# Performance work log

Hardware: AMD Instinct MI355X
Metric: run time of the kernel (lower is better)

The kernel has to match this reference:

```python
import jax, jax.numpy as jnp
import numpy as np
import math

# ---- static configuration (matches init_kwargs) ----
METADATA = [64, 48, 32]   # channels per l = 0,1,2
MAX_L = 3                 # order_out
N_BATCH = 32768
fact = math.factorial

def _cg_complex(l1, m1, l2, m2, l3, m3):
    # Clebsch-Gordan coefficient <l1 m1 l2 m2 | l3 m3> via Racah formula
    if m1 + m2 != m3 or l3 < abs(l1 - l2) or l3 > l1 + l2:
        return 0.0
    pre = math.sqrt((2*l3+1) * fact(l1+l2-l3) * fact(l1-l2+l3) * fact(-l1+l2+l3) / fact(l1+l2+l3+1))
    pre *= math.sqrt(fact(l1+m1)*fact(l1-m1)*fact(l2+m2)*fact(l2-m2)*fact(l3+m3)*fact(l3-m3))
    kmin = max(0, l2-l3-m1, l1-l3+m2)
    kmax = min(l1+l2-l3, l1-m1, l2+m2)
    s = 0.0
    for k in range(kmin, kmax+1):
        s += (-1)**k / (fact(k)*fact(l1+l2-l3-k)*fact(l1-m1-k)*fact(l2+m2-k)*fact(l3-l2+m1+k)*fact(l3-l1-m2+k))
    return pre * s

def _U(l):
    # complex->real spherical harmonic change of basis, rows = real m', cols = complex m
    U = np.zeros((2*l+1, 2*l+1), dtype=np.complex128)
    for m in range(-l, l+1):
        r = m + l
        if m > 0:
            U[r, m+l] = (-1)**m / math.sqrt(2.0); U[r, -m+l] = 1.0/math.sqrt(2.0)
        elif m == 0:
            U[r, l] = 1.0
        else:
            U[r, m+l] = 1j/math.sqrt(2.0); U[r, -m+l] = -1j*(-1)**m/math.sqrt(2.0)
    return U

def _real_cg(l1, l2, l3):
    Cc = np.zeros((2*l1+1, 2*l2+1, 2*l3+1))
    for m1 in range(-l1, l1+1):
        for m2 in range(-l2, l2+1):
            for m3 in range(-l3, l3+1):
                Cc[m1+l1, m2+l2, m3+l3] = _cg_complex(l1, m1, l2, m2, l3, m3)
    T = np.einsum('am,bn,co,mno->abc', _U(l1), _U(l2), _U(l3).conj(), Cc.astype(np.complex128))
    T = T.imag if np.abs(T.imag).max() > np.abs(T.real).max() else T.real
    return np.ascontiguousarray(T).astype(np.float32)

# ---- static index structures ----
L_IN = len(METADATA)
OFF_IN = np.concatenate([[0], np.cumsum([METADATA[l]*(2*l+1) for l in range(L_IN)])]).astype(np.int64)
DIM_IN = int(OFF_IN[-1])  # 368
PATHS = []
for l1 in range(L_IN):
    for l2 in range(L_IN):
        for l3 in range(abs(l1-l2), min(l1+l2, MAX_L)+1):
            PATHS.append((l1, l2, l3, min(METADATA[l1], METADATA[l2])))
MD_OV = [0]*(MAX_L+1)
for (_, _, l3, ch) in PATHS:
    MD_OV[l3] = max(MD_OV[l3], ch)
OFF_OUT = np.concatenate([[0], np.cumsum([MD_OV[l]*(2*l+1) for l in range(MAX_L+1)])]).astype(np.int64)
DIM_OUT = int(OFF_OUT[-1])  # 672
CG = {(l1, l2, l3): jnp.asarray(_real_cg(l1, l2, l3)) for (l1, l2, l3, _) in PATHS}

_mix_id, _scat = [], []
_base = 0
for (l1, l2, l3, ch) in PATHS:
    for i in range(ch):
        for m in range(2*l3+1):
            _mix_id.append(_base + i)
            _scat.append(int(OFF_OUT[l3]) + i*(2*l3+1) + m)
    _base += ch
MIX_ID = jnp.asarray(np.array(_mix_id, dtype=np.int64))
SCATTER = jnp.asarray(np.array(_scat, dtype=np.int64))
N_MIX = _base  # 688

_chan_in = []
_cb = 0
for l in range(L_IN):
    for i in range(METADATA[l]):
        _chan_in += [_cb + i]*(2*l+1)
    _cb += METADATA[l]
CHAN_IN = jnp.asarray(np.array(_chan_in, dtype=np.int64))
N_KEEP = _cb  # 144
_kin, _kout = [], []
for l in range(L_IN):
    cp = min(METADATA[l], MD_OV[l])
    for i in range(cp):
        for m in range(2*l+1):
            _kin.append(int(OFF_IN[l]) + i*(2*l+1) + m)
            _kout.append(int(OFF_OUT[l]) + i*(2*l+1) + m)
KEEP_IN = jnp.asarray(np.array(_kin, dtype=np.int64))
KEEP_OUT = jnp.asarray(np.array(_kout, dtype=np.int64))

SQ3 = math.sqrt(3.0)

def setup_inputs() -> dict:
    key = jax.random.key(0)
    k1, k2, k3 = jax.random.split(key, 3)
    x = jax.random.normal(k1, (N_BATCH, DIM_IN), dtype=jnp.float32)
    keep_coeff = jax.random.uniform(k2, (N_KEEP,), minval=-SQ3, maxval=SQ3, dtype=jnp.float32)
    mix_coeff = jax.random.uniform(k3, (N_MIX,), minval=-SQ3, maxval=SQ3, dtype=jnp.float32)
    return {"x": x, "keep_coeff": keep_coeff, "mix_coeff": mix_coeff}

def reference(x, keep_coeff, mix_coeff):
    n = x.shape[0]
    # keep path: per-channel coeff broadcast over m components
    x_keep = x * keep_coeff[CHAN_IN]  # [N, 368]
    # CG tensor-product self-coupling (diagonal channel pairing per path)
    tps = []
    for (l1, l2, l3, ch) in PATHS:
        x1 = x[:, OFF_IN[l1]:OFF_IN[l1]+ch*(2*l1+1)].reshape(n, ch, 2*l1+1)
        x2 = x[:, OFF_IN[l2]:OFF_IN[l2]+ch*(2*l2+1)].reshape(n, ch, 2*l2+1)
        tps.append(jnp.einsum('nia,nib,abm->nim', x1, x2, CG[(l1, l2, l3)]).reshape(n, -1))
    cat = jnp.concatenate(tps, axis=1)  # [N, 2576] non-overlapped TP output
    cat = cat * 0.5 * mix_coeff[MIX_ID]
    # scatter (index_add) into overlapped output layout
    out = jnp.zeros((n, DIM_OUT), dtype=x.dtype).at[:, SCATTER].add(cat)
    # gather + add of keep path (index_select + add_)
    out = out.at[:, KEEP_OUT].add(x_keep[:, KEEP_IN])
    return out
```

## Files before the change

### kernel.cpp

```cpp
#include <hip/hip_runtime.h>


namespace cgc {

struct cplx { double re, im; };
constexpr cplx cmul(cplx a, cplx b){ return {a.re*b.re - a.im*b.im, a.re*b.im + a.im*b.re}; }

constexpr double cfact(int n){ double r = 1.0; for (int i = 2; i <= n; ++i) r *= i; return r; }
constexpr double cabsd(double x){ return x < 0 ? -x : x; }

constexpr double csqrtd(double x){
  if (x <= 0.0) return 0.0;
  double g = x > 1.0 ? x : 1.0;
  for (int i = 0; i < 48; ++i) g = 0.5*(g + x/g);
  return g;
}

constexpr double SQRT2 = csqrtd(2.0);

constexpr double cg_complex(int l1,int m1,int l2,int m2,int l3,int m3){
  if (m1 + m2 != m3) return 0.0;
  int lo = l1 > l2 ? l1 - l2 : l2 - l1;
  if (l3 < lo || l3 > l1 + l2) return 0.0;
  double pre = csqrtd((2*l3+1) * cfact(l1+l2-l3)*cfact(l1-l2+l3)*cfact(-l1+l2+l3)/cfact(l1+l2+l3+1));
  pre *= csqrtd(cfact(l1+m1)*cfact(l1-m1)*cfact(l2+m2)*cfact(l2-m2)*cfact(l3+m3)*cfact(l3-m3));
  int kmin = 0;
  if (l2-l3-m1 > kmin) kmin = l2-l3-m1;
  if (l1-l3+m2 > kmin) kmin = l1-l3+m2;
  int kmax = l1+l2-l3;
  if (l1-m1 < kmax) kmax = l1-m1;
  if (l2+m2 < kmax) kmax = l2+m2;
  double s = 0.0;
  for (int k = kmin; k <= kmax; ++k){
    double d = cfact(k)*cfact(l1+l2-l3-k)*cfact(l1-m1-k)*cfact(l2+m2-k)
             * cfact(l3-l2+m1+k)*cfact(l3-l1-m2+k);
    s += ((k & 1) ? -1.0 : 1.0) / d;
  }
  return pre * s;
}

constexpr cplx Uent(int l, int r, int c){
  int m = r - l;
  if (m > 0){
    if (c ==  m + l) return { ((m & 1) ? -1.0 : 1.0)/SQRT2, 0.0 };
    if (c == -m + l) return { 1.0/SQRT2, 0.0 };
    return {0.0, 0.0};
  } else if (m == 0){
    if (c == l) return {1.0, 0.0};
    return {0.0, 0.0};
  } else {
    int ma = -m;
    if (c ==  m + l) return { 0.0, 1.0/SQRT2 };
    if (c == -m + l) return { 0.0, -(((ma & 1) ? -1.0 : 1.0))/SQRT2 };
    return {0.0, 0.0};
  }
}

template<int L1,int L2,int L3>
struct CGData { float w[(2*L1+1)*(2*L2+1)*(2*L3+1)]; };

template<int L1,int L2,int L3>
constexpr CGData<L1,L2,L3> make_cg(){
  constexpr int D1 = 2*L1+1, D2 = 2*L2+1, D3 = 2*L3+1;
  cplx U1[D1*D1] = {}; cplx U2[D2*D2] = {}; cplx U3c[D3*D3] = {};
  for (int r = 0; r < D1; ++r) for (int c = 0; c < D1; ++c) U1[r*D1+c] = Uent(L1, r, c);
  for (int r = 0; r < D2; ++r) for (int c = 0; c < D2; ++c) U2[r*D2+c] = Uent(L2, r, c);
  for (int r = 0; r < D3; ++r) for (int c = 0; c < D3; ++c){
    cplx u = Uent(L3, r, c); u.im = -u.im; U3c[r*D3+c] = u;
  }
  double Cc[D1*D2*D3] = {};
  for (int m1 = -L1; m1 <= L1; ++m1)
    for (int m2 = -L2; m2 <= L2; ++m2){
      int m3 = m1 + m2;
      if (m3 < -L3 || m3 > L3) continue;
      Cc[((m1+L1)*D2 + (m2+L2))*D3 + (m3+L3)] = cg_complex(L1,m1,L2,m2,L3,m3);
    }
  double re[D1*D2*D3] = {}; double im[D1*D2*D3] = {};
  for (int a = 0; a < D1; ++a)
    for (int b = 0; b < D2; ++b)
      for (int c = 0; c < D3; ++c){
        double sre = 0.0, sim = 0.0;
        for (int m = 0; m < D1; ++m)
          for (int n = 0; n < D2; ++n){
            int o = m + n - L1 - L2 + L3;
            if (o < 0 || o >= D3) continue;
            double cc = Cc[(m*D2+n)*D3 + o];
            if (cc == 0.0) continue;
            cplx p = cmul(cmul(U1[a*D1+m], U2[b*D2+n]), U3c[c*D3+o]);
            sre += p.re * cc; sim += p.im * cc;
          }
        re[(a*D2+b)*D3+c] = sre; im[(a*D2+b)*D3+c] = sim;
      }
  double mre = 0.0, mim = 0.0;
  for (int k = 0; k < D1*D2*D3; ++k){
    if (cabsd(re[k]) > mre) mre = cabsd(re[k]);
    if (cabsd(im[k]) > mim) mim = cabsd(im[k]);
  }
  CGData<L1,L2,L3> outv{};
  for (int k = 0; k < D1*D2*D3; ++k){
    double v = (mim > mre) ? im[k] : re[k];
    outv.w[k] = (cabsd(v) < 1e-10) ? 0.0f : (float)v;
  }
  return outv;
}

}

template<int L1,int L2,int L3>
__device__ __forceinline__ void tp_path(const float* xa, const float* xb, float cmix, float* acc){
  constexpr cgc::CGData<L1,L2,L3> cg = cgc::make_cg<L1,L2,L3>();
  constexpr int D1 = 2*L1+1, D2 = 2*L2+1, D3 = 2*L3+1;
  #pragma unroll
  for (int a = 0; a < D1; ++a){
    #pragma unroll
    for (int b = 0; b < D2; ++b){
      const float pr = xa[a] * xb[b];
      #pragma unroll
      for (int m = 0; m < D3; ++m){
        const float W = cg.w[(a*D2+b)*D3 + m];
        if (W != 0.0f) acc[m] += (cmix * W) * pr;
      }
    }
  }
}


#define ROWS_PER_BLOCK 4

__global__ __launch_bounds__(256) void selfmix_kernel(
    const float* __restrict__ x, const float* __restrict__ keep,
    const float* __restrict__ mix, float* __restrict__ out, int n)
{
  __shared__ __align__(16) float xs[ROWS_PER_BLOCK * 368];
  __shared__ __align__(16) float os[ROWS_PER_BLOCK * 672];

  const int t = threadIdx.x;
  const long long blk  = blockIdx.x;
  const long long row0 = blk * ROWS_PER_BLOCK;

  {
    const long long nf4_in   = (long long)n * 92;
    const long long base_in  = blk * (ROWS_PER_BLOCK * 92);
    const float4* __restrict__ src = (const float4*)x;
    float4* dst = (float4*)xs;
    if (base_in + t < nf4_in)               dst[t]       = src[base_in + t];
    if (t < 112 && base_in + 256 + t < nf4_in) dst[256+t] = src[base_in + 256 + t];
  }
  __syncthreads();

  if (t < 128){
    const int rowL = t >> 5;
    const int i    = t & 31;
    if (row0 + rowL < n){
      const float* xr = xs + rowL*368;
      float*     orow = os + rowL*672;
      float s = xr[i];
      float p[3], d[5];
      #pragma unroll
      for (int k = 0; k < 3; ++k) p[k] = xr[64 + i*3 + k];
      #pragma unroll
      for (int k = 0; k < 5; ++k) d[k] = xr[208 + i*5 + k];

      float o0 = 0.f;
      float o1[3] = {0.f,0.f,0.f};
      float o2[5] = {0.f,0.f,0.f,0.f,0.f};
      float o3[7] = {0.f,0.f,0.f,0.f,0.f,0.f,0.f};

      tp_path<0,0,0>(&s,&s, 0.5f*mix[  0+i], &o0);
      tp_path<0,1,1>(&s, p, 0.5f*mix[ 64+i],  o1);
      tp_path<0,2,2>(&s, d, 0.5f*mix[112+i],  o2);
      tp_path<1,0,1>( p,&s, 0.5f*mix[144+i],  o1);
      tp_path<1,1,0>( p, p, 0.5f*mix[192+i], &o0);
      tp_path<1,1,1>( p, p, 0.5f*mix[240+i],  o1);
      tp_path<1,1,2>( p, p, 0.5f*mix[288+i],  o2);
      tp_path<1,2,1>( p, d, 0.5f*mix[336+i],  o1);
      tp_path<1,2,2>( p, d, 0.5f*mix[368+i],  o2);
      tp_path<1,2,3>( p, d, 0.5f*mix[400+i],  o3);
      tp_path<2,0,2>( d,&s, 0.5f*mix[432+i],  o2);
      tp_path<2,1,1>( d, p, 0.5f*mix[464+i],  o1);
      tp_path<2,1,2>( d, p, 0.5f*mix[496+i],  o2);
      tp_path<2,1,3>( d, p, 0.5f*mix[528+i],  o3);
      tp_path<2,2,0>( d, d, 0.5f*mix[560+i], &o0);
      tp_path<2,2,1>( d, d, 0.5f*mix[592+i],  o1);
      tp_path<2,2,2>( d, d, 0.5f*mix[624+i],  o2);
      tp_path<2,2,3>( d, d, 0.5f*mix[656+i],  o3);

      o0 += keep[i] * s;
      const float k1 = keep[64+i], k2 = keep[112+i];
      #pragma unroll
      for (int k = 0; k < 3; ++k) o1[k] += k1 * p[k];
      #pragma unroll
      for (int k = 0; k < 5; ++k) o2[k] += k2 * d[k];

      orow[i] = o0;
      #pragma unroll
      for (int k = 0; k < 3; ++k) orow[ 64 + i*3 + k] = o1[k];
      #pragma unroll
      for (int k = 0; k < 5; ++k) orow[208 + i*5 + k] = o2[k];
      #pragma unroll
      for (int k = 0; k < 7; ++k) orow[448 + i*7 + k] = o3[k];
    }
  } else if (t < 192){
    const int rowL = (t - 128) >> 4;
    const int i    = 32 + (t & 15);
    if (row0 + rowL < n){
      const float* xr = xs + rowL*368;
      float*     orow = os + rowL*672;
      float s = xr[i];
      float p[3];
      #pragma unroll
      for (int k = 0; k < 3; ++k) p[k] = xr[64 + i*3 + k];

      float o0 = 0.f;
      float o1[3] = {0.f,0.f,0.f};
      float o2[5] = {0.f,0.f,0.f,0.f,0.f};

      tp_path<0,0,0>(&s,&s, 0.5f*mix[  0+i], &o0);
      tp_path<0,1,1>(&s, p, 0.5f*mix[ 64+i],  o1);
      tp_path<1,0,1>( p,&s, 0.5f*mix[144+i],  o1);
      tp_path<1,1,0>( p, p, 0.5f*mix[192+i], &o0);
      tp_path<1,1,1>( p, p, 0.5f*mix[240+i],  o1);
      tp_path<1,1,2>( p, p, 0.5f*mix[288+i],  o2);

      o0 += keep[i] * s;
      const float k1 = keep[64+i];
      #pragma unroll
      for (int k = 0; k < 3; ++k) o1[k] += k1 * p[k];

      orow[i] = o0;
      #pragma unroll
      for (int k = 0; k < 3; ++k) orow[ 64 + i*3 + k] = o1[k];
      #pragma unroll
      for (int k = 0; k < 5; ++k) orow[208 + i*5 + k] = o2[k];
    }
  } else {
    const int rowL = (t - 192) >> 4;
    const int i    = 48 + (t & 15);
    if (row0 + rowL < n){
      const float* xr = xs + rowL*368;
      float s = xr[i];
      float o0 = 0.f;
      tp_path<0,0,0>(&s,&s, 0.5f*mix[0+i], &o0);
      o0 += keep[i] * s;
      os[rowL*672 + i] = o0;
    }
  }
  __syncthreads();

  {
    const long long nf4_out  = (long long)n * 168;
    const long long base_out = blk * (ROWS_PER_BLOCK * 168);
    const float4* srco = (const float4*)os;
    float4* __restrict__ dsto = (float4*)out;
    if (base_out + t < nf4_out)                 dsto[base_out + t]       = srco[t];
    if (base_out + 256 + t < nf4_out)           dsto[base_out + 256 + t] = srco[256+t];
    if (t < 160 && base_out + 512 + t < nf4_out) dsto[base_out + 512 + t] = srco[512+t];
  }
}

extern "C" void kernel_launch(void* const* d_in, const int* in_sizes, int n_in,
                              void* d_out, int out_size, void* d_ws, size_t ws_size,
                              hipStream_t stream)
{
  const float* x    = (const float*)d_in[0];
  const float* keep = (const float*)d_in[1];
  const float* mix  = (const float*)d_in[2];
  float* out = (float*)d_out;
  const int n = in_sizes[0] / 368;
  const int blocks = (n + ROWS_PER_BLOCK - 1) / ROWS_PER_BLOCK;
  selfmix_kernel<<<blocks, 256, 0, stream>>>(x, keep, mix, out, n);
}
```

Baseline: 147.3 us.

## Process eight rows per block with balanced thread roles and factored mix scaling

Each block now handles 8 rows instead of 4. Every thread computes one heavy channel (0-31) of one row, then also takes a lighter channel (32-47 or 48-63), so no thread idles. This replaces the old split where only 128 of 256 threads did the heavy work. tp_path now accumulates CG-weighted products into a temporary and multiplies by the mix coefficient once per output component, cutting multiplies. The cost is larger shared memory per block (about 33KB), which can limit occupancy, and per-thread work grows.

```diff
diff --git a/kernel.cpp b/kernel.cpp
--- a/kernel.cpp
+++ b/kernel.cpp
@@ -110,6 +110,9 @@
 __device__ __forceinline__ void tp_path(const float* xa, const float* xb, float cmix, float* acc){
   constexpr cgc::CGData<L1,L2,L3> cg = cgc::make_cg<L1,L2,L3>();
   constexpr int D1 = 2*L1+1, D2 = 2*L2+1, D3 = 2*L3+1;
+  float tmp[D3];
+  #pragma unroll
+  for (int m = 0; m < D3; ++m) tmp[m] = 0.0f;
   #pragma unroll
   for (int a = 0; a < D1; ++a){
     #pragma unroll
@@ -118,42 +121,45 @@
       #pragma unroll
       for (int m = 0; m < D3; ++m){
         const float W = cg.w[(a*D2+b)*D3 + m];
-        if (W != 0.0f) acc[m] += (cmix * W) * pr;
+        if (W != 0.0f) tmp[m] += W * pr;
       }
     }
   }
-}
-
-
-#define ROWS_PER_BLOCK 4
+  #pragma unroll
+  for (int m = 0; m < D3; ++m) acc[m] += cmix * tmp[m];
+}
+
+
+#define RPB 8
 
 __global__ __launch_bounds__(256) void selfmix_kernel(
     const float* __restrict__ x, const float* __restrict__ keep,
     const float* __restrict__ mix, float* __restrict__ out, int n)
 {
-  __shared__ __align__(16) float xs[ROWS_PER_BLOCK * 368];
-  __shared__ __align__(16) float os[ROWS_PER_BLOCK * 672];
+  __shared__ __align__(16) float xs[RPB * 368];
+  __shared__ __align__(16) float os[RPB * 672];
 
   const int t = threadIdx.x;
   const long long blk  = blockIdx.x;
-  const long long row0 = blk * ROWS_PER_BLOCK;
+  const long long row0 = blk * RPB;
 
   {
-    const long long nf4_in   = (long long)n * 92;
-    const long long base_in  = blk * (ROWS_PER_BLOCK * 92);
-    const float4* __restrict__ src = (const float4*)x;
-    float4* dst = (float4*)xs;
-    if (base_in + t < nf4_in)               dst[t]       = src[base_in + t];
-    if (t < 112 && base_in + 256 + t < nf4_in) dst[256+t] = src[base_in + 256 + t];
+    const long long nf4  = (long long)n * 92;
+    const long long base = row0 * 92;
+    const float4* __restrict__ x4 = (const float4*)x;
+    float4* xs4 = (float4*)xs;
+    if (base + t < nf4)                   xs4[t]       = x4[base + t];
+    if (base + 256 + t < nf4)             xs4[256 + t] = x4[base + 256 + t];
+    if (t < 224 && base + 512 + t < nf4)  xs4[512 + t] = x4[base + 512 + t];
   }
   __syncthreads();
 
-  if (t < 128){
+  {
     const int rowL = t >> 5;
     const int i    = t & 31;
     if (row0 + rowL < n){
-      const float* xr = xs + rowL*368;
-      float*     orow = os + rowL*672;
+      const float* xr = xs + rowL * 368;
+      float*     orw  = os + rowL * 672;
       float s = xr[i];
       float p[3], d[5];
       #pragma unroll
@@ -192,20 +198,22 @@
       #pragma unroll
       for (int k = 0; k < 5; ++k) o2[k] += k2 * d[k];
 
-      orow[i] = o0;
-      #pragma unroll
-      for (int k = 0; k < 3; ++k) orow[ 64 + i*3 + k] = o1[k];
-      #pragma unroll
-      for (int k = 0; k < 5; ++k) orow[208 + i*5 + k] = o2[k];
-      #pragma unroll
-      for (int k = 0; k < 7; ++k) orow[448 + i*7 + k] = o3[k];
-    }
-  } else if (t < 192){
-    const int rowL = (t - 128) >> 4;
+      orw[i] = o0;
+      #pragma unroll
+      for (int k = 0; k < 3; ++k) orw[ 64 + i*3 + k] = o1[k];
+      #pragma unroll
+      for (int k = 0; k < 5; ++k) orw[208 + i*5 + k] = o2[k];
+      #pragma unroll
+      for (int k = 0; k < 7; ++k) orw[448 + i*7 + k] = o3[k];
+    }
+  }
+
+  if (t < 128){
+    const int rowL = t >> 4;
     const int i    = 32 + (t & 15);
     if (row0 + rowL < n){
-      const float* xr = xs + rowL*368;
-      float*     orow = os + rowL*672;
+      const float* xr = xs + rowL * 368;
+      float*     orw  = os + rowL * 672;
       float s = xr[i];
       float p[3];
       #pragma unroll
@@ -227,18 +235,18 @@
       #pragma unroll
       for (int k = 0; k < 3; ++k) o1[k] += k1 * p[k];
 
-      orow[i] = o0;
-      #pragma unroll
-      for (int k = 0; k < 3; ++k) orow[ 64 + i*3 + k] = o1[k];
-      #pragma unroll
-      for (int k = 0; k < 5; ++k) orow[208 + i*5 + k] = o2[k];
+      orw[i] = o0;
+      #pragma unroll
+      for (int k = 0; k < 3; ++k) orw[ 64 + i*3 + k] = o1[k];
+      #pragma unroll
+      for (int k = 0; k < 5; ++k) orw[208 + i*5 + k] = o2[k];
     }
   } else {
-    const int rowL = (t - 192) >> 4;
-    const int i    = 48 + (t & 15);
+    const int t2   = t - 128;
+    const int rowL = t2 >> 4;
+    const int i    = 48 + (t2 & 15);
     if (row0 + rowL < n){
-      const float* xr = xs + rowL*368;
-      float s = xr[i];
+      const float s = xs[rowL*368 + i];
       float o0 = 0.f;
       tp_path<0,0,0>(&s,&s, 0.5f*mix[0+i], &o0);
       o0 += keep[i] * s;
@@ -248,13 +256,17 @@
   __syncthreads();
 
   {
-    const long long nf4_out  = (long long)n * 168;
-    const long long base_out = blk * (ROWS_PER_BLOCK * 168);
-    const float4* srco = (const float4*)os;
-    float4* __restrict__ dsto = (float4*)out;
-    if (base_out + t < nf4_out)                 dsto[base_out + t]       = srco[t];
-    if (base_out + 256 + t < nf4_out)           dsto[base_out + 256 + t] = srco[256+t];
-    if (t < 160 && base_out + 512 + t < nf4_out) dsto[base_out + 512 + t] = srco[512+t];
+    const long long nf4o = (long long)n * 168;
+    const long long base = row0 * 168;
+    const float4* os4 = (const float4*)os;
+    float4* __restrict__ o4 = (float4*)out;
+    #pragma unroll
+    for (int rnd = 0; rnd < 5; ++rnd){
+      const int sidx = rnd*256 + t;
+      if (base + sidx < nf4o) o4[base + sidx] = os4[sidx];
+    }
+    const int sidx = 5*256 + t;
+    if (t < 64 && base + sidx < nf4o) o4[base + sidx] = os4[sidx];
   }
 }
 
@@ -267,6 +279,6 @@
   const float* mix  = (const float*)d_in[2];
   float* out = (float*)d_out;
   const int n = in_sizes[0] / 368;
-  const int blocks = (n + ROWS_PER_BLOCK - 1) / ROWS_PER_BLOCK;
+  const int blocks = (n + RPB - 1) / RPB;
   selfmix_kernel<<<blocks, 256, 0, stream>>>(x, keep, mix, out, n);
 }
```

Result: faster. 131.6 us (-10.6%).
